# Performance work log

Hardware: AMD Instinct MI355X
Metric: run time of the kernel (lower is better)

## Reference

```python
import jax, jax.numpy as jnp
import numpy as np

N = 8192          # num atoms
K = 32            # neighbors per atom (init kwarg k)
CUTOFF = 10.0     # init kwarg cutoff
NUM_MOLS = 128


def setup_inputs() -> dict:
    key = jax.random.key(0)
    k1, k2 = jax.random.split(key)
    pos = jax.random.normal(k1, (N, 3), dtype=jnp.float32)
    batch = jnp.sort(jax.random.randint(k2, (N,), 0, NUM_MOLS)).astype(jnp.int32)
    return {"pos": pos, "batch": batch}


def _pairwise_dist(pos):
    # ||x_i - x_j|| via the gram-matrix expansion; avoids an [N,N,3] intermediate.
    sq_norm = jnp.sum(pos * pos, axis=-1)                     # [N]
    sq = sq_norm[:, None] + sq_norm[None, :] - 2.0 * (pos @ pos.T)  # [N,N]
    sq = jnp.maximum(sq, 0.0)
    # safe sqrt: exact 0 on the diagonal without nan-producing sqrt'(0) in grads
    safe = jnp.where(sq > 0, sq, 1.0)
    return jnp.where(sq > 0, jnp.sqrt(safe), 0.0)


def reference(pos, batch):
    n = pos.shape[0]
    pdist = _pairwise_dist(pos)                               # [N,N]
    rows = jnp.arange(n)
    diag = rows[:, None] == rows[None, :]
    cross = batch[:, None] != batch[None, :]
    outer = pdist > CUTOFF
    mask = diag | cross | outer
    pdist = jnp.where(mask, CUTOFF, pdist)
    neg_w, indices = jax.lax.top_k(-pdist, K)                 # [N,K] each
    rows_e = jnp.broadcast_to(rows[:, None], indices.shape)
    edge_index = jnp.stack([indices.reshape(-1), rows_e.reshape(-1)])  # [2, N*K]
    edge_weight = -neg_w.reshape(-1)                          # [N*K]
    return edge_index, edge_weight
```

## Files before the change

kernel.cpp:

```cpp
#include <hip/hip_runtime.h>


#define CUTOFF_F 10.0f
#define NUM_MOLS 128
#define ROWS_PER_BLOCK 4

__device__ __forceinline__ float readlane_f(float v, int lane) {
    return __int_as_float(__builtin_amdgcn_readlane(__float_as_int(v), lane));
}

__device__ __forceinline__ float dist_v(float4 pr, float4 pc, bool diag) {
    if (diag) return CUTOFF_F;
    float dot = __fadd_rn(__fadd_rn(__fmul_rn(pr.x, pc.x), __fmul_rn(pr.y, pc.y)),
                          __fmul_rn(pr.z, pc.z));
    float sq = __fsub_rn(__fadd_rn(pr.w, pc.w), __fadd_rn(dot, dot));
    sq = fmaxf(sq, 0.0f);
    float d = (sq > 0.0f) ? __fsqrt_rn(sq) : 0.0f;
    return (d > CUTOFF_F) ? CUTOFF_F : d;
}

__device__ __forceinline__ float4 load_pos4(const float* __restrict__ pos, int g) {
    float x = pos[g * 3 + 0];
    float y = pos[g * 3 + 1];
    float z = pos[g * 3 + 2];
    float sq = __fadd_rn(__fadd_rn(__fmul_rn(x, x), __fmul_rn(y, y)), __fmul_rn(z, z));
    return make_float4(x, y, z, sq);
}

__global__ __launch_bounds__(256)
void knn_prepass(const int* __restrict__ batch, int* __restrict__ ms,
                 float* __restrict__ out, int N, int K) {
    const int t = blockIdx.x * blockDim.x + threadIdx.x;
    const int NK = N * K;
    if (t < NK) out[NK + t] = (float)(t / K);
    if (t < N) {
        const int bi = batch[t];
        const int bp = (t == 0) ? -1 : batch[t - 1];
        for (int b = bp + 1; b <= bi; ++b) ms[b] = t;
        if (t == N - 1)
            for (int b = bi + 1; b <= NUM_MOLS; ++b) ms[b] = N;
    }
}

template <int NCH>
__device__ __forceinline__ void row_core_reg(const float* __restrict__ pos,
                                             float4 pr, int n, int lane,
                                             int start, int end, int r,
                                             float* __restrict__ out,
                                             int NK, int K) {
    float v[NCH];
    int   rk[NCH];
#pragma unroll
    for (int j = 0; j < NCH; ++j) {
        const int c = 64 * j + lane;
        v[j]  = (c < n) ? dist_v(pr, load_pos4(pos, start + c), (start + c) == r)
                        : CUTOFF_F;
        rk[j] = 0;
    }
#pragma unroll
    for (int jj = 0; jj < NCH; ++jj) {
        const int base = 64 * jj;
        const int lim  = (NCH == 1) ? n : min(n - base, 64);
#pragma unroll 4
        for (int cc = 0; cc < lim; ++cc) {
            const float vv = readlane_f(v[jj], cc);
            const int   g  = base + cc;
#pragma unroll
            for (int j = 0; j < NCH; ++j) {
                const int c = 64 * j + lane;
                rk[j] += (vv < v[j]) || (vv == v[j] && g < c);
            }
        }
    }
    int m = 0;
#pragma unroll
    for (int j = 0; j < NCH; ++j) {
        const int c = 64 * j + lane;
        m += __popcll(__ballot(c < n && v[j] < CUTOFF_F));
    }
#pragma unroll
    for (int j = 0; j < NCH; ++j) {
        const int c = 64 * j + lane;
        if (c < n && v[j] < CUTOFF_F && rk[j] < K) {
            const int o = r * K + rk[j];
            out[o]          = (float)(start + c);
            out[2 * NK + o] = v[j];
        }
    }
    if (m < K) {
        const int mm = n - m;
        for (int fb = 0; fb < K - m; fb += 64) {
            const int t = fb + lane;
            const bool active = t < (K - m);
            int idx = 0;
            bool found = false;
            if (active) {
                if (t < start)            { idx = t;                      found = true; }
                else if (t - start >= mm) { idx = end + (t - start - mm); found = true; }
            }
            if (__any(active && !found)) {
                int cnt = 0;
#pragma unroll
                for (int jj = 0; jj < NCH; ++jj) {
                    const int base = 64 * jj;
                    const int lim  = min(n - base, 64);
                    for (int cc = 0; cc < lim; ++cc) {
                        if (readlane_f(v[jj], cc) == CUTOFF_F) {
                            if (active && !found && cnt == t - start) {
                                idx = start + base + cc; found = true;
                            }
                            ++cnt;
                        }
                    }
                }
            }
            if (active) {
                const int o = r * K + m + t;
                out[o]          = (float)idx;
                out[2 * NK + o] = CUTOFF_F;
            }
        }
    }
}

__global__ __launch_bounds__(256, 8)
void knn_rows_kernel(const float* __restrict__ pos,
                     const int* __restrict__ batch,
                     const int* __restrict__ ms,
                     float* __restrict__ out,
                     int N, int K) {
    const int w    = threadIdx.x >> 6;
    const int lane = threadIdx.x & 63;
    const int r    = blockIdx.x * ROWS_PER_BLOCK + w;
    if (r >= N) return;
    const int NK = N * K;

    const int b     = batch[r];
    const int start = ms[b];
    const int end   = ms[b + 1];
    const int n     = end - start;

    const float4 pr = load_pos4(pos, r);

    if      (n <= 64)  row_core_reg<1>(pos, pr, n, lane, start, end, r, out, NK, K);
    else if (n <= 128) row_core_reg<2>(pos, pr, n, lane, start, end, r, out, NK, K);
    else if (n <= 192) row_core_reg<3>(pos, pr, n, lane, start, end, r, out, NK, K);
    else if (n <= 256) row_core_reg<4>(pos, pr, n, lane, start, end, r, out, NK, K);
    else {
        int m = 0;
        for (int cb = 0; cb < n; cb += 64) {
            const int c = cb + lane;
            const float v = (c < n)
                ? dist_v(pr, load_pos4(pos, start + c), (start + c) == r) : CUTOFF_F;
            int rk = 0;
            for (int cc = 0; cc < n; ++cc) {
                const float vv = dist_v(pr, load_pos4(pos, start + cc), (start + cc) == r);
                rk += (vv < v) || (vv == v && cc < c);
            }
            if (c < n && v < CUTOFF_F && rk < K) {
                const int o = r * K + rk;
                out[o]          = (float)(start + c);
                out[2 * NK + o] = v;
            }
            m += __popcll(__ballot(c < n && v < CUTOFF_F));
        }
        if (m < K) {
            const int mm = n - m;
            for (int fb = 0; fb < K - m; fb += 64) {
                const int t = fb + lane;
                const bool active = t < (K - m);
                int idx = 0; bool found = false;
                if (active) {
                    if (t < start)            { idx = t;                      found = true; }
                    else if (t - start >= mm) { idx = end + (t - start - mm); found = true; }
                }
                if (__any(active && !found)) {
                    int cnt = 0;
                    for (int cc = 0; cc < n; ++cc) {
                        if (dist_v(pr, load_pos4(pos, start + cc), (start + cc) == r)
                            == CUTOFF_F) {
                            if (active && !found && cnt == t - start) {
                                idx = start + cc; found = true;
                            }
                            ++cnt;
                        }
                    }
                }
                if (active) {
                    const int o = r * K + m + t;
                    out[o]          = (float)idx;
                    out[2 * NK + o] = CUTOFF_F;
                }
            }
        }
    }
}

extern "C" void kernel_launch(void* const* d_in, const int* in_sizes, int n_in,
                              void* d_out, int out_size, void* d_ws, size_t ws_size,
                              hipStream_t stream) {
    const float* pos   = (const float*)d_in[0];
    const int*   batch = (const int*)d_in[1];
    float*       out   = (float*)d_out;
    int*         ms    = (int*)d_ws;

    const int N = in_sizes[1];
    const int K = out_size / (3 * N);

    const int gridA = (N * K + 255) / 256;
    knn_prepass<<<gridA, 256, 0, stream>>>(batch, ms, out, N, K);

    const int gridB = (N + ROWS_PER_BLOCK - 1) / ROWS_PER_BLOCK;
    knn_rows_kernel<<<gridB, 256, 0, stream>>>(pos, batch, ms, out, N, K);
}
```

Baseline: 67.67 us.

## Fuse prepass into row kernel with wave-ballot molecule boundary search

Removes the separate prepass kernel. Each wave now finds its molecule's start and end by ballot over neighbouring batch entries, falling back to a binary search for large molecules, and writes the row-index half of the output itself. This saves one kernel launch and the dependency between the two kernels. In exchange every row performs extra batch reads and ballots to find its segment boundaries.

```diff
diff --git a/kernel.cpp b/kernel.cpp
--- a/kernel.cpp
+++ b/kernel.cpp
@@ -2,11 +2,13 @@
 
 
 #define CUTOFF_F 10.0f
-#define NUM_MOLS 128
 #define ROWS_PER_BLOCK 4
 
 __device__ __forceinline__ float readlane_f(float v, int lane) {
     return __int_as_float(__builtin_amdgcn_readlane(__float_as_int(v), lane));
+}
+__device__ __forceinline__ int readlane_i(int v, int lane) {
+    return __builtin_amdgcn_readlane(v, lane);
 }
 
 __device__ __forceinline__ float dist_v(float4 pr, float4 pc, bool diag) {
@@ -27,21 +29,6 @@
     return make_float4(x, y, z, sq);
 }
 
-__global__ __launch_bounds__(256)
-void knn_prepass(const int* __restrict__ batch, int* __restrict__ ms,
-                 float* __restrict__ out, int N, int K) {
-    const int t = blockIdx.x * blockDim.x + threadIdx.x;
-    const int NK = N * K;
-    if (t < NK) out[NK + t] = (float)(t / K);
-    if (t < N) {
-        const int bi = batch[t];
-        const int bp = (t == 0) ? -1 : batch[t - 1];
-        for (int b = bp + 1; b <= bi; ++b) ms[b] = t;
-        if (t == N - 1)
-            for (int b = bi + 1; b <= NUM_MOLS; ++b) ms[b] = N;
-    }
-}
-
 template <int NCH>
 __device__ __forceinline__ void row_core_reg(const float* __restrict__ pos,
                                              float4 pr, int n, int lane,
@@ -87,6 +74,8 @@
             out[2 * NK + o] = v[j];
         }
     }
+    for (int k2 = lane; k2 < K; k2 += 64)
+        out[NK + r * K + k2] = (float)r;
     if (m < K) {
         const int mm = n - m;
         for (int fb = 0; fb < K - m; fb += 64) {
@@ -124,23 +113,65 @@
 }
 
 __global__ __launch_bounds__(256, 8)
-void knn_rows_kernel(const float* __restrict__ pos,
-                     const int* __restrict__ batch,
-                     const int* __restrict__ ms,
-                     float* __restrict__ out,
-                     int N, int K) {
+void knn_fused_kernel(const float* __restrict__ pos,
+                      const int* __restrict__ batch,
+                      float* __restrict__ out,
+                      int N, int K) {
     const int w    = threadIdx.x >> 6;
     const int lane = threadIdx.x & 63;
     const int r    = blockIdx.x * ROWS_PER_BLOCK + w;
     if (r >= N) return;
     const int NK = N * K;
 
-    const int b     = batch[r];
-    const int start = ms[b];
-    const int end   = ms[b + 1];
-    const int n     = end - start;
-
+    const int iu = r - 63 + lane;
+    const int id = r + 1 + lane;
+    const int au = batch[max(iu, 0)];
+    const int ad = batch[min(id, N - 1)];
     const float4 pr = load_pos4(pos, r);
+
+    const int b = readlane_i(au, 63);
+
+    const unsigned long long mu = __ballot(iu >= 0 && au == b);
+    int start;
+    if (mu != ~0ull) {
+        start = r - __builtin_clzll(~mu) + 1;
+    } else {
+        const int iu2 = r - 127 + lane;
+        const unsigned long long mu2 =
+            __ballot(iu2 >= 0 && batch[max(iu2, 0)] == b);
+        if (mu2 != ~0ull) {
+            start = r - 63 - __builtin_clzll(~mu2);
+        } else if (r - 127 <= 0) {
+            start = 0;
+        } else {
+            int lo = 0, hi = r;
+            while (lo < hi) { int mid = (lo + hi) >> 1;
+                              if (batch[mid] < b) lo = mid + 1; else hi = mid; }
+            start = lo;
+        }
+    }
+
+    const unsigned long long md = __ballot(id < N && ad == b);
+    int end;
+    if (md != ~0ull) {
+        end = r + 1 + __builtin_ctzll(~md);
+    } else {
+        const int id2 = r + 65 + lane;
+        const unsigned long long md2 =
+            __ballot(id2 < N && batch[min(id2, N - 1)] == b);
+        if (md2 != ~0ull) {
+            end = r + 65 + __builtin_ctzll(~md2);
+        } else if (r + 129 >= N) {
+            end = N;
+        } else {
+            int lo = r + 1, hi = N;
+            while (lo < hi) { int mid = (lo + hi) >> 1;
+                              if (batch[mid] < b + 1) lo = mid + 1; else hi = mid; }
+            end = lo;
+        }
+    }
+
+    const int n = end - start;
 
     if      (n <= 64)  row_core_reg<1>(pos, pr, n, lane, start, end, r, out, NK, K);
     else if (n <= 128) row_core_reg<2>(pos, pr, n, lane, start, end, r, out, NK, K);
@@ -164,6 +195,8 @@
             }
             m += __popcll(__ballot(c < n && v < CUTOFF_F));
         }
+        for (int k2 = lane; k2 < K; k2 += 64)
+            out[NK + r * K + k2] = (float)r;
         if (m < K) {
             const int mm = n - m;
             for (int fb = 0; fb < K - m; fb += 64) {
@@ -202,14 +235,10 @@
     const float* pos   = (const float*)d_in[0];
     const int*   batch = (const int*)d_in[1];
     float*       out   = (float*)d_out;
-    int*         ms    = (int*)d_ws;
 
     const int N = in_sizes[1];
     const int K = out_size / (3 * N);
 
-    const int gridA = (N * K + 255) / 256;
-    knn_prepass<<<gridA, 256, 0, stream>>>(batch, ms, out, N, K);
-
-    const int gridB = (N + ROWS_PER_BLOCK - 1) / ROWS_PER_BLOCK;
-    knn_rows_kernel<<<gridB, 256, 0, stream>>>(pos, batch, ms, out, N, K);
-}
+    const int grid = (N + ROWS_PER_BLOCK - 1) / ROWS_PER_BLOCK;
+    knn_fused_kernel<<<grid, 256, 0, stream>>>(pos, batch, out, N, K);
+}
```

After: 66.33 us. 1.02x faster.
